# Kernel tuning notes

Hardware: AMD Instinct MI355X
Metric: run time of the kernel (lower is better)

Reference implementation:

```python
import jax, jax.numpy as jnp
import numpy as np

N_NODES = 50000
BETA = 0.5
NEG_SLOPE = 0.2


def gat_conv(x, src, dst, W, a_src, a_dst, b):
    """Single-head GAT-style conv: gather, attend, softmax-per-dst, scatter-sum."""
    h = x @ W                                   # [N, F]
    as_ = h @ a_src                             # [N]
    ad_ = h @ a_dst                             # [N]
    e = jax.nn.leaky_relu(as_[src] + ad_[dst], NEG_SLOPE)  # [E]
    # numerically stable softmax over incoming edges of each dst node
    m = jax.ops.segment_max(e, dst, num_segments=N_NODES)  # [N]
    ex = jnp.exp(e - m[dst])                    # [E]
    denom = jax.ops.segment_sum(ex, dst, num_segments=N_NODES)  # [N]
    w = ex / denom[dst]                         # [E]
    out = jax.ops.segment_sum(w[:, None] * h[src], dst, num_segments=N_NODES)
    return out + b


def setup_inputs() -> dict:
    key = jax.random.key(0)
    ks = jax.random.split(key, 8)
    F_in, F_out = 64, 64
    x = jax.random.normal(ks[0], (N_NODES, F_in), dtype=jnp.float32)
    edge_index = jax.random.randint(ks[1], (2, 1600000), 0, N_NODES, dtype=jnp.int64)
    W = jax.random.normal(ks[2], (F_in, F_in), dtype=jnp.float32) * (1.0 / np.sqrt(F_in))
    a_src = jax.random.normal(ks[3], (F_in,), dtype=jnp.float32) * (1.0 / np.sqrt(F_in))
    a_dst = jax.random.normal(ks[4], (F_in,), dtype=jnp.float32) * (1.0 / np.sqrt(F_in))
    b = jnp.zeros((F_in,), dtype=jnp.float32)
    fc_w = jax.random.normal(ks[5], (F_in, F_out), dtype=jnp.float32) * (1.0 / np.sqrt(F_in))
    fc_b = jnp.zeros((F_out,), dtype=jnp.float32)
    return {"x": x, "edge_index": edge_index, "W": W, "a_src": a_src,
            "a_dst": a_dst, "b": b, "fc_w": fc_w, "fc_b": fc_b}


def reference(x, edge_index, W, a_src, a_dst, b, fc_w, fc_b):
    src, dst = edge_index[0], edge_index[1]
    x1 = BETA * gat_conv(x, src, dst, W, a_src, a_dst, b) + (1.0 - BETA) * x
    x2 = BETA * gat_conv(x1, src, dst, W, a_src, a_dst, b) + (1.0 - BETA) * x
    x3 = BETA * gat_conv(x2, src, dst, W, a_src, a_dst, b) + (1.0 - BETA) * x
    h = x3
    out = x3 @ fc_w + fc_b
    return (out, h)
```

## Files before the change

### kernel.cpp

```cpp
#include <hip/hip_runtime.h>
#include <hip/hip_bf16.h>
#include <math.h>

#define N_NODES 50000
#define FDIM 64
#define BETA 0.5f
#define NEG_SLOPE 0.2f

typedef __attribute__((ext_vector_type(8))) short bf16x8;
typedef __attribute__((ext_vector_type(4))) float f32x4;

__device__ __forceinline__ unsigned short f2bf(float f) {
    unsigned u = __float_as_uint(f);
    unsigned r = (u + 0x7FFFu + ((u >> 16) & 1u)) >> 16;
    return (unsigned short)r;
}
__device__ __forceinline__ float bf2f(unsigned short s) {
    return __uint_as_float((unsigned)s << 16);
}

#define CHUNK 4096
__global__ __launch_bounds__(256) void scatter_pairs(
    const unsigned int* __restrict__ eiu, int* __restrict__ gCursor,
    unsigned int* __restrict__ pairs, int E, int CAP) {
    __shared__ int det;
    __shared__ unsigned int staged[CHUNK];
    __shared__ unsigned short tmpd[CHUNK];
    __shared__ int hist[256], sc[256], lbase[256], gbase[256], lcur[256];
    int t = threadIdx.x;
    if (t == 0) det = 0;
    hist[t] = 0;
    __syncthreads();
    int beg = blockIdx.x * CHUNK;
    int end = min(E, beg + CHUNK);
    int n = end - beg;
    {
        int idx = beg + t;
        if (idx < E && eiu[2 * idx + 1] != 0u) atomicOr(&det, 1);
    }
    __syncthreads();
    bool is32 = det != 0;
    for (int i = beg + t; i < end; i += 256) {
        int d = is32 ? (int)eiu[E + i] : (int)eiu[2 * (size_t)(E + i)];
        tmpd[i - beg] = (unsigned short)d;
        atomicAdd(&hist[d >> 8], 1);
    }
    __syncthreads();
    sc[t] = hist[t];
    __syncthreads();
    for (int off = 1; off < 256; off <<= 1) {
        int v = (t >= off) ? sc[t - off] : 0;
        __syncthreads();
        sc[t] += v;
        __syncthreads();
    }
    int excl = sc[t] - hist[t];
    lbase[t] = excl;
    lcur[t] = excl;
    if (hist[t] > 0) gbase[t] = t * CAP + atomicAdd(&gCursor[t], hist[t]);
    __syncthreads();
    for (int i = beg + t; i < end; i += 256) {
        unsigned s = is32 ? eiu[i] : eiu[2 * (size_t)i];
        unsigned td = tmpd[i - beg];
        int b = (int)(td >> 8);
        int lp = atomicAdd(&lcur[b], 1);
        staged[lp] = s | (td << 16);
    }
    __syncthreads();
    for (int j = t; j < n; j += 256) {
        unsigned w = staged[j];
        int b = (int)(w >> 24);
        pairs[gbase[b] + (j - lbase[b])] = w;
    }
}

__global__ __launch_bounds__(1024) void bucket_sort(
    const unsigned int* __restrict__ pairs, const int* __restrict__ gCursor,
    int* __restrict__ offsets, int* __restrict__ srcs, int N, int E, int CAP) {
    __shared__ int scb[256], cnt[256], sc[256], lcur[256];
    __shared__ unsigned short sorted16[16384];
    int b = blockIdx.x, t = threadIdx.x;
    if (t < 256) scb[t] = gCursor[t];
    __syncthreads();
    for (int off = 1; off < 256; off <<= 1) {
        int v = (t < 256 && t >= off) ? scb[t - off] : 0;
        __syncthreads();
        if (t < 256) scb[t] += v;
        __syncthreads();
    }
    int cntb = gCursor[b];
    int beg = scb[b] - cntb;
    int pbase = b * CAP;
    bool useLds = cntb <= 16384;
    if (b == 0 && t == 0) offsets[N] = E;
    if (t < 256) cnt[t] = 0;
    __syncthreads();
    for (int i = t; i < cntb; i += 1024) atomicAdd(&cnt[(pairs[pbase + i] >> 16) & 255u], 1);
    __syncthreads();
    if (t < 256) sc[t] = cnt[t];
    __syncthreads();
    for (int off = 1; off < 256; off <<= 1) {
        int v = (t < 256 && t >= off) ? sc[t - off] : 0;
        __syncthreads();
        if (t < 256) sc[t] += v;
        __syncthreads();
    }
    if (t < 256) {
        int excl = sc[t] - cnt[t];
        int node = (b << 8) + t;
        if (node < N) offsets[node] = beg + excl;
        lcur[t] = excl;
    }
    __syncthreads();
    if (useLds) {
        for (int i = t; i < cntb; i += 1024) {
            unsigned p = pairs[pbase + i];
            int lp = atomicAdd(&lcur[(p >> 16) & 255u], 1);
            sorted16[lp] = (unsigned short)(p & 0xFFFFu);
        }
        __syncthreads();
        for (int j = t; j < cntb; j += 1024) srcs[beg + j] = (int)sorted16[j];
    } else {
        for (int i = t; i < cntb; i += 1024) {
            unsigned p = pairs[pbase + i];
            int lp = atomicAdd(&lcur[(p >> 16) & 255u], 1);
            srcs[beg + lp] = (int)(p & 0xFFFFu);
        }
    }
}

__global__ __launch_bounds__(256) void prep_weights(
    const float* __restrict__ W, const float* __restrict__ fcw,
    unsigned short* __restrict__ WTh, unsigned short* __restrict__ WTl,
    unsigned short* __restrict__ FTh, unsigned short* __restrict__ FTl) {
    for (int idx = blockIdx.x * 256 + threadIdx.x; idx < 4096; idx += gridDim.x * 256) {
        int k = idx >> 6, f = idx & 63;
        float w = W[idx];
        unsigned short hi = f2bf(w);
        WTh[f * 64 + k] = hi;
        WTl[f * 64 + k] = f2bf(w - bf2f(hi));
        float w2 = fcw[idx];
        unsigned short hi2 = f2bf(w2);
        FTh[f * 64 + k] = hi2;
        FTl[f * 64 + k] = f2bf(w2 - bf2f(hi2));
    }
}

__global__ __launch_bounds__(256, 4) void transform_mfma(
    const float* __restrict__ x,
    const unsigned short* __restrict__ WTh, const unsigned short* __restrict__ WTl,
    const float* __restrict__ a_src, const float* __restrict__ a_dst,
    const float* __restrict__ bias,
    unsigned short* __restrict__ hb,
    float* __restrict__ fout,
    float* __restrict__ as_, float* __restrict__ ad_, int N) {
    __shared__ __align__(16) unsigned short WThs[64 * 72];
    __shared__ __align__(16) unsigned short WTls[64 * 72];
    int tid = threadIdx.x;
    {
        int row = tid >> 2;
        int ch = (tid & 3) * 16;
        uint4 h0 = ((const uint4*)(WTh + row * 64 + ch))[0];
        uint4 h1 = ((const uint4*)(WTh + row * 64 + ch))[1];
        uint4 l0 = ((const uint4*)(WTl + row * 64 + ch))[0];
        uint4 l1 = ((const uint4*)(WTl + row * 64 + ch))[1];
        *((uint4*)(WThs + row * 72 + ch)) = h0;
        *((uint4*)(WThs + row * 72 + ch + 8)) = h1;
        *((uint4*)(WTls + row * 72 + ch)) = l0;
        *((uint4*)(WTls + row * 72 + ch + 8)) = l1;
    }

    int wid = tid >> 6;
    int lane = tid & 63;
    int col = lane & 15;
    int quad = lane >> 4;
    int mbase = blockIdx.x * 64 + wid * 16;

    bf16x8 Ah[2], Al[2];
    int arow = mbase + col;
    const float* xr = x + (size_t)(arow < N ? arow : 0) * FDIM + quad * 8;
#pragma unroll
    for (int ks = 0; ks < 2; ks++) {
        float4 xa = *(const float4*)(xr + ks * 32);
        float4 xb = *(const float4*)(xr + ks * 32 + 4);
        float xv[8] = {xa.x, xa.y, xa.z, xa.w, xb.x, xb.y, xb.z, xb.w};
#pragma unroll
        for (int e = 0; e < 8; e++) {
            unsigned short hi = f2bf(xv[e]);
            Ah[ks][e] = (short)hi;
            Al[ks][e] = (short)f2bf(xv[e] - bf2f(hi));
        }
    }
    __syncthreads();

    f32x4 acc[4];
#pragma unroll
    for (int ft = 0; ft < 4; ft++) acc[ft] = (f32x4){0.f, 0.f, 0.f, 0.f};

#pragma unroll
    for (int ft = 0; ft < 4; ft++) {
        int f = ft * 16 + col;
#pragma unroll
        for (int ks = 0; ks < 2; ks++) {
            int off = f * 72 + ks * 32 + quad * 8;
            bf16x8 Bh = *(const bf16x8*)(WThs + off);
            bf16x8 Bl = *(const bf16x8*)(WTls + off);
            acc[ft] = __builtin_amdgcn_mfma_f32_16x16x32_bf16(Ah[ks], Bh, acc[ft], 0, 0, 0);
            acc[ft] = __builtin_amdgcn_mfma_f32_16x16x32_bf16(Ah[ks], Bl, acc[ft], 0, 0, 0);
            acc[ft] = __builtin_amdgcn_mfma_f32_16x16x32_bf16(Al[ks], Bh, acc[ft], 0, 0, 0);
        }
    }

    if (fout) {
#pragma unroll
        for (int ft = 0; ft < 4; ft++) {
            int f = ft * 16 + col;
            float bv = bias ? bias[f] : 0.f;
#pragma unroll
            for (int r = 0; r < 4; r++) {
                int node = mbase + quad * 4 + r;
                if (node < N) fout[(size_t)node * FDIM + f] = acc[ft][r] + bv;
            }
        }
    }
    if (hb) {
#pragma unroll
        for (int ft = 0; ft < 4; ft++) {
            int f = ft * 16 + col;
#pragma unroll
            for (int r = 0; r < 4; r++) {
                int node = mbase + quad * 4 + r;
                if (node < N) hb[(size_t)node * FDIM + f] = f2bf(acc[ft][r]);
            }
        }
    }
    if (as_) {
        float asv[4], adv[4];
#pragma unroll
        for (int ft = 0; ft < 4; ft++) {
            asv[ft] = a_src[ft * 16 + col];
            adv[ft] = a_dst[ft * 16 + col];
        }
#pragma unroll
        for (int r = 0; r < 4; r++) {
            float pa = 0.f, pd = 0.f;
#pragma unroll
            for (int ft = 0; ft < 4; ft++) {
                pa = fmaf(acc[ft][r], asv[ft], pa);
                pd = fmaf(acc[ft][r], adv[ft], pd);
            }
#pragma unroll
            for (int off = 1; off <= 8; off <<= 1) {
                pa += __shfl_xor(pa, off, 64);
                pd += __shfl_xor(pd, off, 64);
            }
            int node = mbase + quad * 4 + r;
            if (col == 0 && node < N) { as_[node] = pa; ad_[node] = pd; }
        }
    }
}

__device__ __forceinline__ void fma8(float* acc, float ex, const uint4& hv) {
    acc[0] = fmaf(ex, __uint_as_float(hv.x << 16), acc[0]);
    acc[1] = fmaf(ex, __uint_as_float(hv.x & 0xFFFF0000u), acc[1]);
    acc[2] = fmaf(ex, __uint_as_float(hv.y << 16), acc[2]);
    acc[3] = fmaf(ex, __uint_as_float(hv.y & 0xFFFF0000u), acc[3]);
    acc[4] = fmaf(ex, __uint_as_float(hv.z << 16), acc[4]);
    acc[5] = fmaf(ex, __uint_as_float(hv.z & 0xFFFF0000u), acc[5]);
    acc[6] = fmaf(ex, __uint_as_float(hv.w << 16), acc[6]);
    acc[7] = fmaf(ex, __uint_as_float(hv.w & 0xFFFF0000u), acc[7]);
}

__global__ __launch_bounds__(256) void gat_gather(
    const unsigned short* __restrict__ hb,
    const float* __restrict__ as_, const float* __restrict__ ad_,
    const int* __restrict__ offsets, const int* __restrict__ srcs,
    const float* __restrict__ bvec, const float* __restrict__ x0,
    float* __restrict__ xout, int N) {
    int wid = (blockIdx.x * blockDim.x + threadIdx.x) >> 6;
    if (wid >= N) return;
    int lane = threadIdx.x & 63;
    int q = lane & 7;
    int eslot = lane >> 3;
    int beg = offsets[wid], end = offsets[wid + 1];
    float adv = ad_[wid];

    float acc[8];
#pragma unroll
    for (int k = 0; k < 8; k++) acc[k] = 0.f;
    float denom = 0.f;
    const unsigned short* hq = hb + (q << 3);

#define LRELU_EXP(E_) __expf((E_) > 0.f ? (E_) : NEG_SLOPE * (E_))
#define NTL(P_) __builtin_nontemporal_load(P_)

    int i = beg + eslot;
    for (; i + 24 < end; i += 32) {
        int s0 = NTL(srcs + i);
        int s1 = NTL(srcs + i + 8);
        int s2 = NTL(srcs + i + 16);
        int s3 = NTL(srcs + i + 24);
        uint4 hv0 = *(const uint4*)(hq + ((size_t)s0 << 6));
        uint4 hv1 = *(const uint4*)(hq + ((size_t)s1 << 6));
        uint4 hv2 = *(const uint4*)(hq + ((size_t)s2 << 6));
        uint4 hv3 = *(const uint4*)(hq + ((size_t)s3 << 6));
        float e0 = as_[s0] + adv;
        float e1 = as_[s1] + adv;
        float e2 = as_[s2] + adv;
        float e3 = as_[s3] + adv;
        float ex0 = LRELU_EXP(e0);
        float ex1 = LRELU_EXP(e1);
        float ex2 = LRELU_EXP(e2);
        float ex3 = LRELU_EXP(e3);
        denom += (ex0 + ex1) + (ex2 + ex3);
        fma8(acc, ex0, hv0);
        fma8(acc, ex1, hv1);
        fma8(acc, ex2, hv2);
        fma8(acc, ex3, hv3);
    }
    for (; i + 8 < end; i += 16) {
        int s0 = NTL(srcs + i);
        int s1 = NTL(srcs + i + 8);
        uint4 hv0 = *(const uint4*)(hq + ((size_t)s0 << 6));
        uint4 hv1 = *(const uint4*)(hq + ((size_t)s1 << 6));
        float e0 = as_[s0] + adv;
        float e1 = as_[s1] + adv;
        float ex0 = LRELU_EXP(e0);
        float ex1 = LRELU_EXP(e1);
        denom += ex0 + ex1;
        fma8(acc, ex0, hv0);
        fma8(acc, ex1, hv1);
    }
    for (; i < end; i += 8) {
        int s0 = NTL(srcs + i);
        uint4 hv0 = *(const uint4*)(hq + ((size_t)s0 << 6));
        float e0 = as_[s0] + adv;
        float ex0 = LRELU_EXP(e0);
        denom += ex0;
        fma8(acc, ex0, hv0);
    }
#undef LRELU_EXP

#pragma unroll
    for (int off = 8; off <= 32; off <<= 1) {
        denom += __shfl_xor(denom, off, 64);
#pragma unroll
        for (int k = 0; k < 8; k++) acc[k] += __shfl_xor(acc[k], off, 64);
    }
    if (lane < 8) {
        float inv = denom > 0.f ? 1.f / denom : 0.f;
        int fb = lane * 8;
        f32x4 b0 = *(const f32x4*)(bvec + fb);
        f32x4 b1 = *(const f32x4*)(bvec + fb + 4);
        f32x4 x0a = NTL((const f32x4*)(x0 + (size_t)wid * FDIM + fb));
        f32x4 x0b = NTL((const f32x4*)(x0 + (size_t)wid * FDIM + fb + 4));
        f32x4 o0, o1;
        o0.x = BETA * (acc[0] * inv + b0.x) + (1.f - BETA) * x0a.x;
        o0.y = BETA * (acc[1] * inv + b0.y) + (1.f - BETA) * x0a.y;
        o0.z = BETA * (acc[2] * inv + b0.z) + (1.f - BETA) * x0a.z;
        o0.w = BETA * (acc[3] * inv + b0.w) + (1.f - BETA) * x0a.w;
        o1.x = BETA * (acc[4] * inv + b1.x) + (1.f - BETA) * x0b.x;
        o1.y = BETA * (acc[5] * inv + b1.y) + (1.f - BETA) * x0b.y;
        o1.z = BETA * (acc[6] * inv + b1.z) + (1.f - BETA) * x0b.z;
        o1.w = BETA * (acc[7] * inv + b1.w) + (1.f - BETA) * x0b.w;
        __builtin_nontemporal_store(o0, (f32x4*)(xout + (size_t)wid * FDIM + fb));
        __builtin_nontemporal_store(o1, (f32x4*)(xout + (size_t)wid * FDIM + fb + 4));
    }
#undef NTL
}

extern "C" void kernel_launch(void* const* d_in, const int* in_sizes, int n_in,
                              void* d_out, int out_size, void* d_ws, size_t ws_size,
                              hipStream_t stream) {
    const int N = N_NODES;
    const int E = in_sizes[1] / 2;
    const int NB = (N + 255) >> 8;
    const int CAP = (((E / N) * 256) * 2 + 1023) & ~1023;

    const float* x     = (const float*)d_in[0];
    const void*  ei    = d_in[1];
    const float* W     = (const float*)d_in[2];
    const float* a_src = (const float*)d_in[3];
    const float* a_dst = (const float*)d_in[4];
    const float* bvec  = (const float*)d_in[5];
    const float* fc_w  = (const float*)d_in[6];
    const float* fc_b  = (const float*)d_in[7];

    float* out = (float*)d_out;
    float* x3  = out + (size_t)N * FDIM;

    char* p = (char*)d_ws;
    auto alloc = [&](size_t bytes) -> void* {
        void* r = (void*)p;
        p += (bytes + 255) & ~(size_t)255;
        return r;
    };
    int*            gCursor  = (int*)alloc(256 * 4);
    unsigned int*   pairs    = (unsigned int*)alloc((size_t)256 * CAP * 4);
    int*            srcs     = (int*)alloc((size_t)E * 4);
    int*            offsets  = (int*)alloc((size_t)(N + 1) * 4);
    float*          as_      = (float*)alloc((size_t)N * 4);
    float*          ad_      = (float*)alloc((size_t)N * 4);
    unsigned short* hbuf     = (unsigned short*)alloc((size_t)N * FDIM * 2);
    float*          xbuf     = (float*)alloc((size_t)N * FDIM * 4);
    unsigned short* WTh      = (unsigned short*)alloc(4096 * 2);
    unsigned short* WTl      = (unsigned short*)alloc(4096 * 2);
    unsigned short* FTh      = (unsigned short*)alloc(4096 * 2);
    unsigned short* FTl      = (unsigned short*)alloc(4096 * 2);

    hipMemsetAsync(gCursor, 0, 256 * 4, stream);

    prep_weights<<<16, 256, 0, stream>>>(W, fc_w, WTh, WTl, FTh, FTl);

    scatter_pairs<<<(E + CHUNK - 1) / CHUNK, 256, 0, stream>>>(
        (const unsigned int*)ei, gCursor, pairs, E, CAP);
    bucket_sort<<<NB, 1024, 0, stream>>>(pairs, gCursor, offsets, srcs, N, E, CAP);

    int tgrid = (N + 63) / 64;
    int ggrid = (N * 64 + 255) / 256;

    transform_mfma<<<tgrid, 256, 0, stream>>>(x, WTh, WTl, a_src, a_dst, nullptr,
                                              hbuf, nullptr, as_, ad_, N);
    gat_gather<<<ggrid, 256, 0, stream>>>(hbuf, as_, ad_, offsets, srcs, bvec, x, xbuf, N);
    transform_mfma<<<tgrid, 256, 0, stream>>>(xbuf, WTh, WTl, a_src, a_dst, nullptr,
                                              hbuf, nullptr, as_, ad_, N);
    gat_gather<<<ggrid, 256, 0, stream>>>(hbuf, as_, ad_, offsets, srcs, bvec, x, xbuf, N);
    transform_mfma<<<tgrid, 256, 0, stream>>>(xbuf, WTh, WTl, a_src, a_dst, nullptr,
                                              hbuf, nullptr, as_, ad_, N);
    gat_gather<<<ggrid, 256, 0, stream>>>(hbuf, as_, ad_, offsets, srcs, bvec, x, x3, N);
    transform_mfma<<<tgrid, 256, 0, stream>>>(x3, FTh, FTl, nullptr, nullptr, fc_b,
                                              nullptr, out, nullptr, nullptr, N);
}
```

Baseline: 270.6 us.

## Process eight degree-sorted nodes per wavefront in GAT gather

Adds a degree histogram, scan and scatter to build a permutation of nodes sorted by in-degree. The gather kernel now gives each 8-lane group its own destination node, so a wavefront handles 8 nodes with similar degrees and loops up to their maximum degree, with predicated loads. This removes the cross-lane shuffle reduction and the idle lanes on low-degree nodes. In exchange it adds three small kernels and uses scattered node order for the x0 and xout accesses. Each lane group now reads consecutive srcs entries, so srcs loads are less coalesced.

```diff
diff --git a/kernel.cpp b/kernel.cpp
--- a/kernel.cpp
+++ b/kernel.cpp
@@ -126,6 +126,44 @@
             int lp = atomicAdd(&lcur[(p >> 16) & 255u], 1);
             srcs[beg + lp] = (int)(p & 0xFFFFu);
         }
+    }
+}
+
+__global__ __launch_bounds__(256) void deg_hist(
+    const int* __restrict__ offsets, int* __restrict__ degCnt, int N) {
+    __shared__ int h[256];
+    h[threadIdx.x] = 0;
+    __syncthreads();
+    for (int i = blockIdx.x * blockDim.x + threadIdx.x; i < N; i += gridDim.x * blockDim.x) {
+        int d = offsets[i + 1] - offsets[i];
+        atomicAdd(&h[min(d, 255)], 1);
+    }
+    __syncthreads();
+    if (h[threadIdx.x]) atomicAdd(&degCnt[threadIdx.x], h[threadIdx.x]);
+}
+
+__global__ __launch_bounds__(256) void deg_scan(int* degCnt) {
+    __shared__ int sc[256];
+    int t = threadIdx.x;
+    int c = degCnt[t];
+    sc[t] = c;
+    __syncthreads();
+    for (int off = 1; off < 256; off <<= 1) {
+        int v = (t >= off) ? sc[t - off] : 0;
+        __syncthreads();
+        sc[t] += v;
+        __syncthreads();
+    }
+    degCnt[t] = sc[t] - c;
+}
+
+__global__ __launch_bounds__(256) void deg_scatter(
+    const int* __restrict__ offsets, int* __restrict__ degCnt,
+    int* __restrict__ perm, int N) {
+    for (int i = blockIdx.x * blockDim.x + threadIdx.x; i < N; i += gridDim.x * blockDim.x) {
+        int d = min(offsets[i + 1] - offsets[i], 255);
+        int slot = atomicAdd(&degCnt[d], 1);
+        perm[slot] = i;
     }
 }
 
@@ -275,15 +313,23 @@
     const unsigned short* __restrict__ hb,
     const float* __restrict__ as_, const float* __restrict__ ad_,
     const int* __restrict__ offsets, const int* __restrict__ srcs,
+    const int* __restrict__ perm,
     const float* __restrict__ bvec, const float* __restrict__ x0,
     float* __restrict__ xout, int N) {
     int wid = (blockIdx.x * blockDim.x + threadIdx.x) >> 6;
-    if (wid >= N) return;
     int lane = threadIdx.x & 63;
+    int g = lane >> 3;
     int q = lane & 7;
-    int eslot = lane >> 3;
-    int beg = offsets[wid], end = offsets[wid + 1];
-    float adv = ad_[wid];
+    int ni = wid * 8 + g;
+    bool active = ni < N;
+    int node = active ? perm[ni] : 0;
+    int beg = active ? offsets[node] : 0;
+    int end = active ? offsets[node + 1] : 0;
+    float adv = active ? ad_[node] : 0.f;
+    int mx = end - beg;
+    mx = max(mx, __shfl_xor(mx, 8, 64));
+    mx = max(mx, __shfl_xor(mx, 16, 64));
+    mx = max(mx, __shfl_xor(mx, 32, 64));
 
     float acc[8];
 #pragma unroll
@@ -292,14 +338,18 @@
     const unsigned short* hq = hb + (q << 3);
 
 #define LRELU_EXP(E_) __expf((E_) > 0.f ? (E_) : NEG_SLOPE * (E_))
-#define NTL(P_) __builtin_nontemporal_load(P_)
-
-    int i = beg + eslot;
-    for (; i + 24 < end; i += 32) {
-        int s0 = NTL(srcs + i);
-        int s1 = NTL(srcs + i + 8);
-        int s2 = NTL(srcs + i + 16);
-        int s3 = NTL(srcs + i + 24);
+
+    for (int st = 0; st < mx; st += 4) {
+        int i0 = beg + st;
+        bool v0 = i0 < end, v1 = i0 + 1 < end, v2 = i0 + 2 < end, v3 = i0 + 3 < end;
+        int a0 = v0 ? i0 : 0;
+        int a1 = v1 ? i0 + 1 : 0;
+        int a2 = v2 ? i0 + 2 : 0;
+        int a3 = v3 ? i0 + 3 : 0;
+        int s0 = srcs[a0];
+        int s1 = srcs[a1];
+        int s2 = srcs[a2];
+        int s3 = srcs[a3];
         uint4 hv0 = *(const uint4*)(hq + ((size_t)s0 << 6));
         uint4 hv1 = *(const uint4*)(hq + ((size_t)s1 << 6));
         uint4 hv2 = *(const uint4*)(hq + ((size_t)s2 << 6));
@@ -308,52 +358,26 @@
         float e1 = as_[s1] + adv;
         float e2 = as_[s2] + adv;
         float e3 = as_[s3] + adv;
-        float ex0 = LRELU_EXP(e0);
-        float ex1 = LRELU_EXP(e1);
-        float ex2 = LRELU_EXP(e2);
-        float ex3 = LRELU_EXP(e3);
+        float ex0 = v0 ? LRELU_EXP(e0) : 0.f;
+        float ex1 = v1 ? LRELU_EXP(e1) : 0.f;
+        float ex2 = v2 ? LRELU_EXP(e2) : 0.f;
+        float ex3 = v3 ? LRELU_EXP(e3) : 0.f;
         denom += (ex0 + ex1) + (ex2 + ex3);
         fma8(acc, ex0, hv0);
         fma8(acc, ex1, hv1);
         fma8(acc, ex2, hv2);
         fma8(acc, ex3, hv3);
     }
-    for (; i + 8 < end; i += 16) {
-        int s0 = NTL(srcs + i);
-        int s1 = NTL(srcs + i + 8);
-        uint4 hv0 = *(const uint4*)(hq + ((size_t)s0 << 6));
-        uint4 hv1 = *(const uint4*)(hq + ((size_t)s1 << 6));
-        float e0 = as_[s0] + adv;
-        float e1 = as_[s1] + adv;
-        float ex0 = LRELU_EXP(e0);
-        float ex1 = LRELU_EXP(e1);
-        denom += ex0 + ex1;
-        fma8(acc, ex0, hv0);
-        fma8(acc, ex1, hv1);
-    }
-    for (; i < end; i += 8) {
-        int s0 = NTL(srcs + i);
-        uint4 hv0 = *(const uint4*)(hq + ((size_t)s0 << 6));
-        float e0 = as_[s0] + adv;
-        float ex0 = LRELU_EXP(e0);
-        denom += ex0;
-        fma8(acc, ex0, hv0);
-    }
 #undef LRELU_EXP
 
-#pragma unroll
-    for (int off = 8; off <= 32; off <<= 1) {
-        denom += __shfl_xor(denom, off, 64);
-#pragma unroll
-        for (int k = 0; k < 8; k++) acc[k] += __shfl_xor(acc[k], off, 64);
-    }
-    if (lane < 8) {
+    if (active) {
         float inv = denom > 0.f ? 1.f / denom : 0.f;
-        int fb = lane * 8;
+        int fb = q * 8;
         f32x4 b0 = *(const f32x4*)(bvec + fb);
         f32x4 b1 = *(const f32x4*)(bvec + fb + 4);
-        f32x4 x0a = NTL((const f32x4*)(x0 + (size_t)wid * FDIM + fb));
-        f32x4 x0b = NTL((const f32x4*)(x0 + (size_t)wid * FDIM + fb + 4));
+        const float* x0r = x0 + (size_t)node * FDIM + fb;
+        f32x4 x0a = *(const f32x4*)(x0r);
+        f32x4 x0b = *(const f32x4*)(x0r + 4);
         f32x4 o0, o1;
         o0.x = BETA * (acc[0] * inv + b0.x) + (1.f - BETA) * x0a.x;
         o0.y = BETA * (acc[1] * inv + b0.y) + (1.f - BETA) * x0a.y;
@@ -363,10 +387,10 @@
         o1.y = BETA * (acc[5] * inv + b1.y) + (1.f - BETA) * x0b.y;
         o1.z = BETA * (acc[6] * inv + b1.z) + (1.f - BETA) * x0b.z;
         o1.w = BETA * (acc[7] * inv + b1.w) + (1.f - BETA) * x0b.w;
-        __builtin_nontemporal_store(o0, (f32x4*)(xout + (size_t)wid * FDIM + fb));
-        __builtin_nontemporal_store(o1, (f32x4*)(xout + (size_t)wid * FDIM + fb + 4));
-    }
-#undef NTL
+        float* xr = xout + (size_t)node * FDIM + fb;
+        *(f32x4*)(xr) = o0;
+        *(f32x4*)(xr + 4) = o1;
+    }
 }
 
 extern "C" void kernel_launch(void* const* d_in, const int* in_sizes, int n_in,
@@ -395,10 +419,11 @@
         p += (bytes + 255) & ~(size_t)255;
         return r;
     };
-    int*            gCursor  = (int*)alloc(256 * 4);
+    int*            gCursor  = (int*)alloc(512 * 4);
     unsigned int*   pairs    = (unsigned int*)alloc((size_t)256 * CAP * 4);
     int*            srcs     = (int*)alloc((size_t)E * 4);
     int*            offsets  = (int*)alloc((size_t)(N + 1) * 4);
+    int*            perm     = (int*)alloc((size_t)N * 4);
     float*          as_      = (float*)alloc((size_t)N * 4);
     float*          ad_      = (float*)alloc((size_t)N * 4);
     unsigned short* hbuf     = (unsigned short*)alloc((size_t)N * FDIM * 2);
@@ -407,8 +432,9 @@
     unsigned short* WTl      = (unsigned short*)alloc(4096 * 2);
     unsigned short* FTh      = (unsigned short*)alloc(4096 * 2);
     unsigned short* FTl      = (unsigned short*)alloc(4096 * 2);
-
-    hipMemsetAsync(gCursor, 0, 256 * 4, stream);
+    int* degCnt = gCursor + 256;
+
+    hipMemsetAsync(gCursor, 0, 512 * 4, stream);
 
     prep_weights<<<16, 256, 0, stream>>>(W, fc_w, WTh, WTl, FTh, FTl);
 
@@ -416,18 +442,26 @@
         (const unsigned int*)ei, gCursor, pairs, E, CAP);
     bucket_sort<<<NB, 1024, 0, stream>>>(pairs, gCursor, offsets, srcs, N, E, CAP);
 
+    deg_hist<<<64, 256, 0, stream>>>(offsets, degCnt, N);
+    deg_scan<<<1, 256, 0, stream>>>(degCnt);
+    deg_scatter<<<64, 256, 0, stream>>>(offsets, degCnt, perm, N);
+
     int tgrid = (N + 63) / 64;
-    int ggrid = (N * 64 + 255) / 256;
+    int gwaves = (N + 7) / 8;
+    int ggrid = (gwaves + 3) / 4;
 
     transform_mfma<<<tgrid, 256, 0, stream>>>(x, WTh, WTl, a_src, a_dst, nullptr,
                                               hbuf, nullptr, as_, ad_, N);
-    gat_gather<<<ggrid, 256, 0, stream>>>(hbuf, as_, ad_, offsets, srcs, bvec, x, xbuf, N);
+    gat_gather<<<ggrid, 256, 0, stream>>>(hbuf, as_, ad_, offsets, srcs, perm,
+                                          bvec, x, xbuf, N);
     transform_mfma<<<tgrid, 256, 0, stream>>>(xbuf, WTh, WTl, a_src, a_dst, nullptr,
                                               hbuf, nullptr, as_, ad_, N);
-    gat_gather<<<ggrid, 256, 0, stream>>>(hbuf, as_, ad_, offsets, srcs, bvec, x, xbuf, N);
+    gat_gather<<<ggrid, 256, 0, stream>>>(hbuf, as_, ad_, offsets, srcs, perm,
+                                          bvec, x, xbuf, N);
     transform_mfma<<<tgrid, 256, 0, stream>>>(xbuf, WTh, WTl, a_src, a_dst, nullptr,
                                               hbuf, nullptr, as_, ad_, N);
-    gat_gather<<<ggrid, 256, 0, stream>>>(hbuf, as_, ad_, offsets, srcs, bvec, x, x3, N);
+    gat_gather<<<ggrid, 256, 0, stream>>>(hbuf, as_, ad_, offsets, srcs, perm,
+                                          bvec, x, x3, N);
     transform_mfma<<<tgrid, 256, 0, stream>>>(x3, FTh, FTl, nullptr, nullptr, fc_b,
                                               nullptr, out, nullptr, nullptr, N);
 }
```

After: 347.0 us. 1.28x slower.
